# Performance work log

Measured on AMD Instinct MI355X. Metric: run time of the kernel, lower is better.

## Reference

```python
import jax, jax.numpy as jnp
import numpy as np

GRID = 64
ECC = 10.0
ATT_CTR = (3.0, 0.0)
NORM_SIGMA = 0.5


def _grids():
    coords = jnp.linspace(-ECC, ECC, GRID, dtype=jnp.float32)
    X, Y = jnp.meshgrid(coords, coords)          # (64,64)
    RF_X = X.reshape(-1)                         # (4096,) one RF center per grid point
    RF_Y = Y.reshape(-1)
    return X, Y, RF_X, RF_Y


def _fields(X, Y, RF_X, RF_Y, sigma):
    # Batched Gaussian fields: (64,64,4096), each normalized to unit sum.
    d2 = (X[:, :, None] - RF_X) ** 2 + (Y[:, :, None] - RF_Y) ** 2
    g = jnp.exp(-d2 / (2.0 * sigma ** 2))
    return g / jnp.sum(g, axis=(0, 1), keepdims=True)


def setup_inputs() -> dict:
    key = jax.random.key(0)
    ks = jax.random.split(key, 2)
    stim = jax.random.uniform(ks[0], (GRID, GRID, 256), dtype=jnp.float32)
    return {
        "stim": stim,
        "prf_sigma_scale_factor": jnp.float32(0.2),
        "attention_field_sigma": jnp.float32(2.0),
        "attention_field_gain": jnp.float32(4.0),
        "suppressive_surround_sigma_factor": jnp.float32(3.0),
        "summation_field_sigma_factor": jnp.float32(2.0),
    }


def reference(stim, prf_sigma_scale_factor, attention_field_sigma,
              attention_field_gain, suppressive_surround_sigma_factor,
              summation_field_sigma_factor):
    X, Y, RF_X, RF_Y = _grids()
    if stim.ndim != 3:
        stim = stim[:, :, None]

    # Attention field: unnormalized Gaussian, flattened, gain*g + 1.
    att = jnp.exp(-((X - ATT_CTR[0]) ** 2 + (Y - ATT_CTR[1]) ** 2)
                  / (2.0 * attention_field_sigma ** 2)).reshape(-1)  # (4096,)
    attfield = attention_field_gain * att + 1.0

    rf_sigma = 0.07 + prf_sigma_scale_factor * jnp.sqrt(RF_X ** 2 + RF_Y ** 2)  # (4096,)

    receptive_field = _fields(X, Y, RF_X, RF_Y, rf_sigma)                                  # (64,64,4096)
    suppressive_surround = _fields(X, Y, RF_X, RF_Y, rf_sigma * suppressive_surround_sigma_factor).reshape(GRID * GRID, -1)
    summation_field = _fields(X, Y, RF_X, RF_Y, rf_sigma * summation_field_sigma_factor).reshape(GRID * GRID, -1)

    stimulus_drive = jnp.einsum('ijk,ija->ka', receptive_field, stim)   # (4096, a)
    numerator = stimulus_drive * attfield[:, None]                      # (4096, a)
    surroundresponse = suppressive_surround.T @ numerator               # (4096, a)
    predicted_neural = numerator / (surroundresponse + NORM_SIGMA)
    predicted_voxel = summation_field.T @ predicted_neural
    # voxel_lookup_indices is identity (voxeldata=None), so lookups are no-ops.
    return (numerator, surroundresponse, predicted_neural, predicted_voxel)
```

## Files before the change

kernel.cpp:

```cpp
#include <hip/hip_runtime.h>
#include <hip/hip_bf16.h>
#include <math.h>

#define NP 4096
#define NA 256

typedef unsigned short ushort_t;
typedef __attribute__((ext_vector_type(8))) short short8;
typedef __attribute__((ext_vector_type(4))) float f32x4;
typedef __attribute__((ext_vector_type(8))) unsigned short ushort8v;

__device__ __forceinline__ ushort_t f2bf(float x) {
    __hip_bfloat16 h = __float2bfloat16(x);
    return *reinterpret_cast<ushort_t*>(&h);
}
__device__ __forceinline__ float bf2f(ushort_t u) {
    unsigned x = ((unsigned)u) << 16;
    return __builtin_bit_cast(float, x);
}

__global__ __launch_bounds__(512)
void setup_all(const float* __restrict__ stim,
               const float* __restrict__ pscale,
               const float* __restrict__ pasig,
               const float* __restrict__ pagain,
               const float* __restrict__ pssf,
               const float* __restrict__ psff,
               ushort_t* __restrict__ stimT,
               ushort_t* __restrict__ gxbI,
               float* __restrict__ gy2I,
               float* __restrict__ attI)
{
    __shared__ float lt[64 * 68];
    const int t = threadIdx.x;
    const int bx = blockIdx.x;
    const float step = 20.0f / 63.0f;

    if (bx < 256) {
        const int g0 = (bx & 63) * 64, a0 = (bx >> 6) * 64;
        const int gr = t >> 3, ar = (t & 7) * 8;
        *(f32x4*)&lt[gr * 68 + ar]     = *(const f32x4*)&stim[(size_t)(g0 + gr) * NA + a0 + ar];
        *(f32x4*)&lt[gr * 68 + ar + 4] = *(const f32x4*)&stim[(size_t)(g0 + gr) * NA + a0 + ar + 4];
        __syncthreads();
        const int a = t >> 3, c8 = (t & 7) * 8;
        ushort8v u;
        #pragma unroll
        for (int i = 0; i < 8; ++i) u[i] = f2bf(lt[(c8 + i) * 68 + a]);
        *(ushort8v*)&stimT[(size_t)(a0 + a) * NP + g0 + c8] = u;
    } else {
        const int b    = bx - 256;
        const int f    = b >> 6;
        const int pblk = b & 63;
        const int w    = t >> 6;
        const int l    = t & 63;
        const float sc_scale = pscale[0];
        const float fac = (f == 0) ? 1.0f : (f == 1 ? pssf[0] : psff[0]);
        const float coord = -10.0f + step * (float)l;
        ushort_t* gxb = gxbI + ((size_t)f * 64 + pblk) * 4096;
        float*    gy2 = gy2I + ((size_t)f * 64 + pblk) * 4096;

        #pragma unroll
        for (int i = 0; i < 8; ++i) {
            const int pl = w * 8 + i, p = pblk * 64 + pl;
            float cx = -10.0f + step * (float)(p & 63);
            float cy = -10.0f + step * (float)(p >> 6);
            float sg = (0.07f + sc_scale * sqrtf(cx * cx + cy * cy)) * fac;
            float inv = 1.0f / (2.0f * sg * sg);
            float dx = coord - cx, dy = coord - cy;
            float ex = expf(-dx * dx * inv);
            float ey = expf(-dy * dy * inv);
            float sx = ex, sy = ey;
            #pragma unroll
            for (int o = 32; o > 0; o >>= 1) {
                sx += __shfl_xor(sx, o);
                sy += __shfl_xor(sy, o);
            }
            gxb[pl * 64 + l] = f2bf(ex / sx);
            gy2[l * 64 + (((pl & 15) * 4) ^ ((l & 7) << 3)) + (pl >> 4)] = ey / sy;
            if (f == 0 && l == 0) {
                float asig = pasig[0];
                float d2 = (cx - 3.0f) * (cx - 3.0f) + cy * cy;
                attI[p] = pagain[0] * expf(-d2 / (2.0f * asig * asig)) + 1.0f;
            }
        }
    }
}

template <int MODE>
__global__ __launch_bounds__(512)
void field_gemm(const ushort_t* __restrict__ bT,
                const ushort_t* __restrict__ gxbF,
                const float* __restrict__ gy2F,
                const float* __restrict__ attI,
                const float* __restrict__ num,
                float* __restrict__ C,
                float* __restrict__ C2,
                ushort_t* __restrict__ CT,
                const ushort_t* __restrict__ numTsrc)
{
    __shared__ __align__(16) unsigned char smem[147712];
    ushort_t* lB   = (ushort_t*)smem;
    float*    lgy2 = (float*)(smem + 131072);
    float*    latt = (float*)(smem + 147456);

    const int t    = threadIdx.x;
    const int w    = t >> 6;
    const int l    = t & 63;
    const int asub = w >> 1;
    const int kh   = w & 1;
    const int r16  = l & 15;
    const int q    = l >> 4;
    const int srow  = l >> 3;
    const int sslot = (l & 7) ^ (srow & 7);
    const int base_w = kh * 4096 + asub * 1024;

    const int v    = blockIdx.x;
    const int lid  = (v & 7) * 32 + (v >> 3);
    const int pblk = lid & 63;
    const int p0   = pblk * 64;
    const int a0   = (lid >> 6) * 64;

#define STAGE(buf, tn)                                                         \
    _Pragma("unroll")                                                          \
    for (int h = 0; h < 2; ++h) {                                              \
        const ushort_t* src = bT + (size_t)(a0 + asub * 16 + h * 8 + srow) * NP\
                              + (2 * (tn) + kh) * 64 + sslot * 8;              \
        ushort_t* dst = lB + (buf) * 8192 + base_w + h * 512;                  \
        __builtin_amdgcn_global_load_lds(                                      \
            (const __attribute__((address_space(1))) unsigned int*)src,        \
            (__attribute__((address_space(3))) unsigned int*)dst, 16, 0, 0);   \
    }

    STAGE(0, 0); STAGE(1, 1); STAGE(2, 2);
    STAGE(3, 3); STAGE(4, 4); STAGE(5, 5);

    {
        const float* gsrc = gy2F + (size_t)pblk * 4096;
        #pragma unroll
        for (int r = 0; r < 2; ++r) {
            const float* src = gsrc + (w * 2 + r) * 256 + l * 4;
            float* dst = lgy2 + (w * 2 + r) * 256;
            __builtin_amdgcn_global_load_lds(
                (const __attribute__((address_space(1))) unsigned int*)src,
                (__attribute__((address_space(3))) unsigned int*)dst, 16, 0, 0);
        }
    }
    if (MODE == 0 && w == 0) {
        const float* src = attI + p0 + l;
        __builtin_amdgcn_global_load_lds(
            (const __attribute__((address_space(1))) unsigned int*)src,
            (__attribute__((address_space(3))) unsigned int*)latt, 4, 0, 0);
    }

    const ushort_t* gxb = gxbF + (size_t)pblk * 4096;
    short8 gxf[4][2];
    #pragma unroll
    for (int pt = 0; pt < 4; ++pt) {
        const int row = pt * 16 + r16;
        gxf[pt][0] = *(const short8*)&gxb[row * 64 + q * 8];
        gxf[pt][1] = *(const short8*)&gxb[row * 64 + 32 + q * 8];
    }

    __syncthreads();

    const int bo0 = r16 * 64 + ((q ^ (r16 & 7)) * 8);
    const int bo1 = r16 * 64 + (((4 + q) ^ (r16 & 7)) * 8);

    f32x4 acc[4];
    #pragma unroll
    for (int pt = 0; pt < 4; ++pt) acc[pt] = (f32x4){0.f, 0.f, 0.f, 0.f};

    short8 Aa0, Aa1, Ab0, Ab1;
    f32x4 s4a, s4b;
    {
        const ushort_t* bb0 = lB + base_w;
        Aa0 = *(const short8*)(bb0 + bo0);
        Aa1 = *(const short8*)(bb0 + bo1);
        const int gi0 = kh;
        s4a = *(const f32x4*)(lgy2 + gi0 * 64 + ((r16 * 4) ^ ((gi0 & 7) << 3)));
    }

#define STEP(TT, VM, CA0, CA1, CS4, NA0, NA1, NS4, PRE, ST)                    \
    {                                                                          \
        const int tt_k = (TT);                                                 \
        asm volatile("s_waitcnt vmcnt(" #VM ")" ::: "memory");                 \
        if (PRE) {                                                             \
            const ushort_t* bbn = lB + ((tt_k + 1) & 7) * 8192 + base_w;       \
            NA0 = *(const short8*)(bbn + bo0);                                 \
            NA1 = *(const short8*)(bbn + bo1);                                 \
            const int gin = 2 * (tt_k + 1) + kh;                               \
            NS4 = *(const f32x4*)(lgy2 + gin * 64 +                            \
                                  ((r16 * 4) ^ ((gin & 7) << 3)));             \
        }                                                                      \
        if (ST) { STAGE((tt_k + 6) & 7, tt_k + 6); }                           \
        __builtin_amdgcn_s_setprio(1);                                         \
        _Pragma("unroll")                                                      \
        for (int pt = 0; pt < 4; ++pt) {                                       \
            f32x4 tmp = (f32x4){0.f, 0.f, 0.f, 0.f};                           \
            tmp = __builtin_amdgcn_mfma_f32_16x16x32_bf16(CA0, gxf[pt][0], tmp, 0, 0, 0); \
            tmp = __builtin_amdgcn_mfma_f32_16x16x32_bf16(CA1, gxf[pt][1], tmp, 0, 0, 0); \
            float sc = CS4[pt];                                                \
            acc[pt] += tmp * sc;                                               \
        }                                                                      \
        __builtin_amdgcn_s_setprio(0);                                         \
    }

    #pragma unroll
    for (int pi = 0; pi < 13; ++pi) {
        STEP(2 * pi,     8, Aa0, Aa1, s4a, Ab0, Ab1, s4b, 1, 1);
        STEP(2 * pi + 1, 8, Ab0, Ab1, s4b, Aa0, Aa1, s4a, 1, 1);
    }
    STEP(26, 8, Aa0, Aa1, s4a, Ab0, Ab1, s4b, 1, 0);
    STEP(27, 6, Ab0, Ab1, s4b, Aa0, Aa1, s4a, 1, 0);
    STEP(28, 4, Aa0, Aa1, s4a, Ab0, Ab1, s4b, 1, 0);
    STEP(29, 2, Ab0, Ab1, s4b, Aa0, Aa1, s4a, 1, 0);
    STEP(30, 0, Aa0, Aa1, s4a, Ab0, Ab1, s4b, 1, 0);
    STEP(31, 0, Ab0, Ab1, s4b, Aa0, Aa1, s4a, 0, 0);
#undef STEP
#undef STAGE

    __syncthreads();
    float* lred_ap = (float*)smem;
    float* lred_pa = (float*)(smem + 34816);

    const int a_base = asub * 16 + q * 4;
    #pragma unroll
    for (int pt = 0; pt < 4; ++pt) {
        const int p_idx = pt * 16 + r16;
        *(f32x4*)&lred_pa[(kh * 64 + p_idx) * 68 + a_base] = acc[pt];
        #pragma unroll
        for (int r = 0; r < 4; ++r)
            lred_ap[(kh * 64 + a_base + r) * 68 + p_idx] = acc[pt][r];
    }
    __syncthreads();

    if (MODE != 2) {
        const int aL = t >> 3, p8 = (t & 7) * 8;
        f32x4 s0 = *(f32x4*)&lred_ap[aL * 68 + p8] +
                   *(f32x4*)&lred_ap[(64 + aL) * 68 + p8];
        f32x4 s1 = *(f32x4*)&lred_ap[aL * 68 + p8 + 4] +
                   *(f32x4*)&lred_ap[(64 + aL) * 68 + p8 + 4];
        ushort8v cv;
        if (MODE == 0) {
            f32x4 t0 = *(f32x4*)&latt[p8];
            f32x4 t1 = *(f32x4*)&latt[p8 + 4];
            s0 *= t0; s1 *= t1;
            #pragma unroll
            for (int r = 0; r < 4; ++r) {
                cv[r] = f2bf(s0[r]);
                cv[4 + r] = f2bf(s1[r]);
            }
        } else {
            ushort8v nt = *(const ushort8v*)&numTsrc[(size_t)(a0 + aL) * NP + p0 + p8];
            #pragma unroll
            for (int r = 0; r < 4; ++r) {
                cv[r] = f2bf(bf2f(nt[r]) / (s0[r] + 0.5f));
                cv[4 + r] = f2bf(bf2f(nt[4 + r]) / (s1[r] + 0.5f));
            }
        }
        *(ushort8v*)&CT[(size_t)(a0 + aL) * NP + p0 + p8] = cv;
    }

    {
        const int pL = t >> 3, a8 = (t & 7) * 8;
        f32x4 s0 = *(f32x4*)&lred_pa[pL * 68 + a8] +
                   *(f32x4*)&lred_pa[(64 + pL) * 68 + a8];
        f32x4 s1 = *(f32x4*)&lred_pa[pL * 68 + a8 + 4] +
                   *(f32x4*)&lred_pa[(64 + pL) * 68 + a8 + 4];
        float* cbase = C + (size_t)(p0 + pL) * NA + a0 + a8;
        if (MODE == 0) {
            float att = latt[pL];
            s0 *= att; s1 *= att;
            *(f32x4*)cbase = s0;
            *(f32x4*)(cbase + 4) = s1;
        } else if (MODE == 1) {
            *(f32x4*)cbase = s0;
            *(f32x4*)(cbase + 4) = s1;
            const float* nb = num + (size_t)(p0 + pL) * NA + a0 + a8;
            f32x4 n0 = *(const f32x4*)nb;
            f32x4 n1 = *(const f32x4*)(nb + 4);
            f32x4 o0 = n0 / (s0 + 0.5f);
            f32x4 o1 = n1 / (s1 + 0.5f);
            float* c2 = C2 + (size_t)(p0 + pL) * NA + a0 + a8;
            *(f32x4*)c2 = o0;
            *(f32x4*)(c2 + 4) = o1;
        } else {
            *(f32x4*)cbase = s0;
            *(f32x4*)(cbase + 4) = s1;
        }
    }
}

extern "C" void kernel_launch(void* const* d_in, const int* in_sizes, int n_in,
                              void* d_out, int out_size, void* d_ws, size_t ws_size,
                              hipStream_t stream)
{
    const float* stim   = (const float*)d_in[0];
    const float* pscale = (const float*)d_in[1];
    const float* pasig  = (const float*)d_in[2];
    const float* pagain = (const float*)d_in[3];
    const float* pssf   = (const float*)d_in[4];
    const float* psff   = (const float*)d_in[5];

    float* out  = (float*)d_out;
    float* num  = out;
    float* surr = out + (size_t)NP * NA;
    float* pn   = out + 2 * (size_t)NP * NA;
    float* pv   = out + 3 * (size_t)NP * NA;

    ushort_t* stimT = (ushort_t*)d_ws;
    ushort_t* numT  = stimT + (size_t)NA * NP;
    ushort_t* pnT   = numT + (size_t)NA * NP;
    ushort_t* gxbI  = pnT + (size_t)NA * NP;
    float*    gy2I  = (float*)(gxbI + (size_t)3 * 64 * 4096);
    float*    attI  = gy2I + (size_t)3 * 64 * 4096;

    setup_all<<<448, 512, 0, stream>>>(stim, pscale, pasig, pagain, pssf, psff,
                                       stimT, gxbI, gy2I, attI);

    const ushort_t* gx0 = gxbI;
    const ushort_t* gx1 = gxbI + (size_t)64 * 4096;
    const ushort_t* gx2 = gxbI + (size_t)128 * 4096;
    const float*    gy0 = gy2I;
    const float*    gy1 = gy2I + (size_t)64 * 4096;
    const float*    gy2 = gy2I + (size_t)128 * 4096;

    field_gemm<0><<<256, 512, 0, stream>>>(stimT, gx0, gy0, attI, nullptr,
                                           num, nullptr, numT, nullptr);
    field_gemm<1><<<256, 512, 0, stream>>>(numT, gx1, gy1, attI, num,
                                           surr, pn, pnT, numT);
    field_gemm<2><<<256, 512, 0, stream>>>(pnT, gx2, gy2, attI, nullptr,
                                           pv, nullptr, nullptr, nullptr);
}
```

Measured before the change: 57.42 us.

## Split K four ways across 16 waves per block in field GEMM

Doubles the field_gemm block to 1024 threads so that four wave groups split the 4096-long reduction instead of two, each running 16 pipeline steps instead of 32. The staging ring shrinks from 8 buffers to 4 larger ones with a prefetch depth of 3, and the LDS reduction now sums four partial tiles, with each thread writing 4-wide outputs. The aim is more latency hiding and a shorter serial K loop per wave, since only 256 blocks are launched. The cost is a shallower prefetch pipeline, a larger cross-wave reduction, and more register and LDS pressure under the 1024-thread launch bound.

```diff
diff --git a/kernel.cpp b/kernel.cpp
--- a/kernel.cpp
+++ b/kernel.cpp
@@ -8,6 +8,7 @@
 typedef unsigned short ushort_t;
 typedef __attribute__((ext_vector_type(8))) short short8;
 typedef __attribute__((ext_vector_type(4))) float f32x4;
+typedef __attribute__((ext_vector_type(4))) unsigned short ushort4v;
 typedef __attribute__((ext_vector_type(8))) unsigned short ushort8v;
 
 __device__ __forceinline__ ushort_t f2bf(float x) {
@@ -87,7 +88,7 @@
 }
 
 template <int MODE>
-__global__ __launch_bounds__(512)
+__global__ __launch_bounds__(1024)
 void field_gemm(const ushort_t* __restrict__ bT,
                 const ushort_t* __restrict__ gxbF,
                 const float* __restrict__ gy2F,
@@ -106,13 +107,13 @@
     const int t    = threadIdx.x;
     const int w    = t >> 6;
     const int l    = t & 63;
-    const int asub = w >> 1;
-    const int kh   = w & 1;
+    const int asub = w >> 2;
+    const int kq   = w & 3;
     const int r16  = l & 15;
     const int q    = l >> 4;
     const int srow  = l >> 3;
     const int sslot = (l & 7) ^ (srow & 7);
-    const int base_w = kh * 4096 + asub * 1024;
+    const int base_w = kq * 4096 + asub * 1024;
 
     const int v    = blockIdx.x;
     const int lid  = (v & 7) * 32 + (v >> 3);
@@ -124,26 +125,21 @@
     _Pragma("unroll")                                                          \
     for (int h = 0; h < 2; ++h) {                                              \
         const ushort_t* src = bT + (size_t)(a0 + asub * 16 + h * 8 + srow) * NP\
-                              + (2 * (tn) + kh) * 64 + sslot * 8;              \
-        ushort_t* dst = lB + (buf) * 8192 + base_w + h * 512;                  \
+                              + (4 * (tn) + kq) * 64 + sslot * 8;              \
+        ushort_t* dst = lB + (buf) * 16384 + base_w + h * 512;                 \
         __builtin_amdgcn_global_load_lds(                                      \
             (const __attribute__((address_space(1))) unsigned int*)src,        \
             (__attribute__((address_space(3))) unsigned int*)dst, 16, 0, 0);   \
     }
 
     STAGE(0, 0); STAGE(1, 1); STAGE(2, 2);
-    STAGE(3, 3); STAGE(4, 4); STAGE(5, 5);
 
     {
-        const float* gsrc = gy2F + (size_t)pblk * 4096;
-        #pragma unroll
-        for (int r = 0; r < 2; ++r) {
-            const float* src = gsrc + (w * 2 + r) * 256 + l * 4;
-            float* dst = lgy2 + (w * 2 + r) * 256;
-            __builtin_amdgcn_global_load_lds(
-                (const __attribute__((address_space(1))) unsigned int*)src,
-                (__attribute__((address_space(3))) unsigned int*)dst, 16, 0, 0);
-        }
+        const float* src = gy2F + (size_t)pblk * 4096 + w * 256 + l * 4;
+        float* dst = lgy2 + w * 256;
+        __builtin_amdgcn_global_load_lds(
+            (const __attribute__((address_space(1))) unsigned int*)src,
+            (__attribute__((address_space(3))) unsigned int*)dst, 16, 0, 0);
     }
     if (MODE == 0 && w == 0) {
         const float* src = attI + p0 + l;
@@ -176,7 +172,7 @@
         const ushort_t* bb0 = lB + base_w;
         Aa0 = *(const short8*)(bb0 + bo0);
         Aa1 = *(const short8*)(bb0 + bo1);
-        const int gi0 = kh;
+        const int gi0 = kq;
         s4a = *(const f32x4*)(lgy2 + gi0 * 64 + ((r16 * 4) ^ ((gi0 & 7) << 3)));
     }
 
@@ -185,14 +181,14 @@
         const int tt_k = (TT);                                                 \
         asm volatile("s_waitcnt vmcnt(" #VM ")" ::: "memory");                 \
         if (PRE) {                                                             \
-            const ushort_t* bbn = lB + ((tt_k + 1) & 7) * 8192 + base_w;       \
+            const ushort_t* bbn = lB + ((tt_k + 1) & 3) * 16384 + base_w;      \
             NA0 = *(const short8*)(bbn + bo0);                                 \
             NA1 = *(const short8*)(bbn + bo1);                                 \
-            const int gin = 2 * (tt_k + 1) + kh;                               \
+            const int gin = 4 * (tt_k + 1) + kq;                               \
             NS4 = *(const f32x4*)(lgy2 + gin * 64 +                            \
                                   ((r16 * 4) ^ ((gin & 7) << 3)));             \
         }                                                                      \
-        if (ST) { STAGE((tt_k + 6) & 7, tt_k + 6); }                           \
+        if (ST) { STAGE((tt_k + 3) & 3, tt_k + 3); }                           \
         __builtin_amdgcn_s_setprio(1);                                         \
         _Pragma("unroll")                                                      \
         for (int pt = 0; pt < 4; ++pt) {                                       \
@@ -206,87 +202,69 @@
     }
 
     #pragma unroll
-    for (int pi = 0; pi < 13; ++pi) {
-        STEP(2 * pi,     8, Aa0, Aa1, s4a, Ab0, Ab1, s4b, 1, 1);
-        STEP(2 * pi + 1, 8, Ab0, Ab1, s4b, Aa0, Aa1, s4a, 1, 1);
-    }
-    STEP(26, 8, Aa0, Aa1, s4a, Ab0, Ab1, s4b, 1, 0);
-    STEP(27, 6, Ab0, Ab1, s4b, Aa0, Aa1, s4a, 1, 0);
-    STEP(28, 4, Aa0, Aa1, s4a, Ab0, Ab1, s4b, 1, 0);
-    STEP(29, 2, Ab0, Ab1, s4b, Aa0, Aa1, s4a, 1, 0);
-    STEP(30, 0, Aa0, Aa1, s4a, Ab0, Ab1, s4b, 1, 0);
-    STEP(31, 0, Ab0, Ab1, s4b, Aa0, Aa1, s4a, 0, 0);
+    for (int pi = 0; pi < 6; ++pi) {
+        STEP(2 * pi,     2, Aa0, Aa1, s4a, Ab0, Ab1, s4b, 1, 1);
+        STEP(2 * pi + 1, 2, Ab0, Ab1, s4b, Aa0, Aa1, s4a, 1, 1);
+    }
+    STEP(12, 2, Aa0, Aa1, s4a, Ab0, Ab1, s4b, 1, 1);
+    STEP(13, 2, Ab0, Ab1, s4b, Aa0, Aa1, s4a, 1, 0);
+    STEP(14, 0, Aa0, Aa1, s4a, Ab0, Ab1, s4b, 1, 0);
+    STEP(15, 0, Ab0, Ab1, s4b, Aa0, Aa1, s4a, 0, 0);
 #undef STEP
 #undef STAGE
 
     __syncthreads();
-    float* lred_ap = (float*)smem;
-    float* lred_pa = (float*)(smem + 34816);
+    float* lred_pa = (float*)smem;
+    float* lred_ap = (float*)(smem + 69632);
 
     const int a_base = asub * 16 + q * 4;
     #pragma unroll
     for (int pt = 0; pt < 4; ++pt) {
         const int p_idx = pt * 16 + r16;
-        *(f32x4*)&lred_pa[(kh * 64 + p_idx) * 68 + a_base] = acc[pt];
+        *(f32x4*)&lred_pa[(kq * 64 + p_idx) * 68 + a_base] = acc[pt];
         #pragma unroll
         for (int r = 0; r < 4; ++r)
-            lred_ap[(kh * 64 + a_base + r) * 68 + p_idx] = acc[pt][r];
+            lred_ap[(kq * 64 + a_base + r) * 68 + p_idx] = acc[pt][r];
     }
     __syncthreads();
 
     if (MODE != 2) {
-        const int aL = t >> 3, p8 = (t & 7) * 8;
-        f32x4 s0 = *(f32x4*)&lred_ap[aL * 68 + p8] +
-                   *(f32x4*)&lred_ap[(64 + aL) * 68 + p8];
-        f32x4 s1 = *(f32x4*)&lred_ap[aL * 68 + p8 + 4] +
-                   *(f32x4*)&lred_ap[(64 + aL) * 68 + p8 + 4];
-        ushort8v cv;
+        const int aL = t >> 4, p4 = (t & 15) * 4;
+        f32x4 s0 = *(f32x4*)&lred_ap[aL * 68 + p4] +
+                   *(f32x4*)&lred_ap[(64 + aL) * 68 + p4] +
+                   *(f32x4*)&lred_ap[(128 + aL) * 68 + p4] +
+                   *(f32x4*)&lred_ap[(192 + aL) * 68 + p4];
+        ushort4v cv;
         if (MODE == 0) {
-            f32x4 t0 = *(f32x4*)&latt[p8];
-            f32x4 t1 = *(f32x4*)&latt[p8 + 4];
-            s0 *= t0; s1 *= t1;
+            s0 *= *(f32x4*)&latt[p4];
             #pragma unroll
-            for (int r = 0; r < 4; ++r) {
-                cv[r] = f2bf(s0[r]);
-                cv[4 + r] = f2bf(s1[r]);
-            }
+            for (int r = 0; r < 4; ++r) cv[r] = f2bf(s0[r]);
         } else {
-            ushort8v nt = *(const ushort8v*)&numTsrc[(size_t)(a0 + aL) * NP + p0 + p8];
+            ushort4v nt = *(const ushort4v*)&numTsrc[(size_t)(a0 + aL) * NP + p0 + p4];
             #pragma unroll
-            for (int r = 0; r < 4; ++r) {
+            for (int r = 0; r < 4; ++r)
                 cv[r] = f2bf(bf2f(nt[r]) / (s0[r] + 0.5f));
-                cv[4 + r] = f2bf(bf2f(nt[4 + r]) / (s1[r] + 0.5f));
-            }
         }
-        *(ushort8v*)&CT[(size_t)(a0 + aL) * NP + p0 + p8] = cv;
+        *(ushort4v*)&CT[(size_t)(a0 + aL) * NP + p0 + p4] = cv;
     }
 
     {
-        const int pL = t >> 3, a8 = (t & 7) * 8;
-        f32x4 s0 = *(f32x4*)&lred_pa[pL * 68 + a8] +
-                   *(f32x4*)&lred_pa[(64 + pL) * 68 + a8];
-        f32x4 s1 = *(f32x4*)&lred_pa[pL * 68 + a8 + 4] +
-                   *(f32x4*)&lred_pa[(64 + pL) * 68 + a8 + 4];
-        float* cbase = C + (size_t)(p0 + pL) * NA + a0 + a8;
+        const int pL = t >> 4, a4 = (t & 15) * 4;
+        f32x4 s0 = *(f32x4*)&lred_pa[pL * 68 + a4] +
+                   *(f32x4*)&lred_pa[(64 + pL) * 68 + a4] +
+                   *(f32x4*)&lred_pa[(128 + pL) * 68 + a4] +
+                   *(f32x4*)&lred_pa[(192 + pL) * 68 + a4];
+        float* cbase = C + (size_t)(p0 + pL) * NA + a0 + a4;
         if (MODE == 0) {
-            float att = latt[pL];
-            s0 *= att; s1 *= att;
+            s0 *= latt[pL];
             *(f32x4*)cbase = s0;
-            *(f32x4*)(cbase + 4) = s1;
         } else if (MODE == 1) {
             *(f32x4*)cbase = s0;
-            *(f32x4*)(cbase + 4) = s1;
-            const float* nb = num + (size_t)(p0 + pL) * NA + a0 + a8;
-            f32x4 n0 = *(const f32x4*)nb;
-            f32x4 n1 = *(const f32x4*)(nb + 4);
+            f32x4 n0 = *(const f32x4*)(num + (size_t)(p0 + pL) * NA + a0 + a4);
             f32x4 o0 = n0 / (s0 + 0.5f);
-            f32x4 o1 = n1 / (s1 + 0.5f);
-            float* c2 = C2 + (size_t)(p0 + pL) * NA + a0 + a8;
-            *(f32x4*)c2 = o0;
-            *(f32x4*)(c2 + 4) = o1;
+            *(f32x4*)(C2 + (size_t)(p0 + pL) * NA + a0 + a4) = o0;
         } else {
             *(f32x4*)cbase = s0;
-            *(f32x4*)(cbase + 4) = s1;
         }
     }
 }
@@ -325,10 +303,10 @@
     const float*    gy1 = gy2I + (size_t)64 * 4096;
     const float*    gy2 = gy2I + (size_t)128 * 4096;
 
-    field_gemm<0><<<256, 512, 0, stream>>>(stimT, gx0, gy0, attI, nullptr,
-                                           num, nullptr, numT, nullptr);
-    field_gemm<1><<<256, 512, 0, stream>>>(numT, gx1, gy1, attI, num,
-                                           surr, pn, pnT, numT);
-    field_gemm<2><<<256, 512, 0, stream>>>(pnT, gx2, gy2, attI, nullptr,
-                                           pv, nullptr, nullptr, nullptr);
-}
+    field_gemm<0><<<256, 1024, 0, stream>>>(stimT, gx0, gy0, attI, nullptr,
+                                            num, nullptr, numT, nullptr);
+    field_gemm<1><<<256, 1024, 0, stream>>>(numT, gx1, gy1, attI, num,
+                                            surr, pn, pnT, numT);
+    field_gemm<2><<<256, 1024, 0, stream>>>(pnT, gx2, gy2, attI, nullptr,
+                                            pv, nullptr, nullptr, nullptr);
+}
```

After: 61.57 us. +7.2%, slower.

## Load B operand directly from global into registers, drop LDS staging ring

Applied to the files above, without the earlier changes.

Replaces the 8-buffer LDS ring fed by global_load_lds with direct per-lane global loads of the bT operand into a 4-deep register rotation consumed by the MFMAs. This removes the LDS write/read traffic, the manual vmcnt waits and one barrier, and shrinks shared memory from about 148KB to 86KB, which could allow more resident blocks. In exchange each lane issues strided global loads with less prefetch depth, so latency hiding now depends on the compiler's scheduling and on the cache.

```diff
diff --git a/kernel.cpp b/kernel.cpp
--- a/kernel.cpp
+++ b/kernel.cpp
@@ -98,10 +98,11 @@
                 ushort_t* __restrict__ CT,
                 const ushort_t* __restrict__ numTsrc)
 {
-    __shared__ __align__(16) unsigned char smem[147712];
-    ushort_t* lB   = (ushort_t*)smem;
-    float*    lgy2 = (float*)(smem + 131072);
-    float*    latt = (float*)(smem + 147456);
+    __shared__ __align__(16) unsigned char smem[86272];
+    float* lred_ap = (float*)smem;
+    float* lred_pa = (float*)(smem + 34816);
+    float* lgy2    = (float*)(smem + 69632);
+    float* latt    = (float*)(smem + 86016);
 
     const int t    = threadIdx.x;
     const int w    = t >> 6;
@@ -110,29 +111,12 @@
     const int kh   = w & 1;
     const int r16  = l & 15;
     const int q    = l >> 4;
-    const int srow  = l >> 3;
-    const int sslot = (l & 7) ^ (srow & 7);
-    const int base_w = kh * 4096 + asub * 1024;
 
     const int v    = blockIdx.x;
     const int lid  = (v & 7) * 32 + (v >> 3);
     const int pblk = lid & 63;
     const int p0   = pblk * 64;
     const int a0   = (lid >> 6) * 64;
-
-#define STAGE(buf, tn)                                                         \
-    _Pragma("unroll")                                                          \
-    for (int h = 0; h < 2; ++h) {                                              \
-        const ushort_t* src = bT + (size_t)(a0 + asub * 16 + h * 8 + srow) * NP\
-                              + (2 * (tn) + kh) * 64 + sslot * 8;              \
-        ushort_t* dst = lB + (buf) * 8192 + base_w + h * 512;                  \
-        __builtin_amdgcn_global_load_lds(                                      \
-            (const __attribute__((address_space(1))) unsigned int*)src,        \
-            (__attribute__((address_space(3))) unsigned int*)dst, 16, 0, 0);   \
-    }
-
-    STAGE(0, 0); STAGE(1, 1); STAGE(2, 2);
-    STAGE(3, 3); STAGE(4, 4); STAGE(5, 5);
 
     {
         const float* gsrc = gy2F + (size_t)pblk * 4096;
@@ -161,38 +145,34 @@
         gxf[pt][1] = *(const short8*)&gxb[row * 64 + 32 + q * 8];
     }
 
+    const ushort_t* gbase = bT + (size_t)(a0 + asub * 16 + r16) * NP + q * 8;
+#define GLOAD(D0, D1, TT) {                                                    \
+        const int goff = (2 * (TT) + kh) * 64;                                 \
+        D0 = *(const short8*)(gbase + goff);                                   \
+        D1 = *(const short8*)(gbase + goff + 32); }
+
+    short8 pa0, pa1, pb0, pb1, pc0, pc1, pd0, pd1;
+    GLOAD(pa0, pa1, 0); GLOAD(pb0, pb1, 1);
+    GLOAD(pc0, pc1, 2); GLOAD(pd0, pd1, 3);
+
     __syncthreads();
-
-    const int bo0 = r16 * 64 + ((q ^ (r16 & 7)) * 8);
-    const int bo1 = r16 * 64 + (((4 + q) ^ (r16 & 7)) * 8);
 
     f32x4 acc[4];
     #pragma unroll
     for (int pt = 0; pt < 4; ++pt) acc[pt] = (f32x4){0.f, 0.f, 0.f, 0.f};
 
-    short8 Aa0, Aa1, Ab0, Ab1;
     f32x4 s4a, s4b;
-    {
-        const ushort_t* bb0 = lB + base_w;
-        Aa0 = *(const short8*)(bb0 + bo0);
-        Aa1 = *(const short8*)(bb0 + bo1);
-        const int gi0 = kh;
+    {   const int gi0 = kh;
         s4a = *(const f32x4*)(lgy2 + gi0 * 64 + ((r16 * 4) ^ ((gi0 & 7) << 3)));
     }
 
-#define STEP(TT, VM, CA0, CA1, CS4, NA0, NA1, NS4, PRE, ST)                    \
+#define STEP(TT, CA0, CA1, CS4, NS4, PRE, LD)                                  \
     {                                                                          \
-        const int tt_k = (TT);                                                 \
-        asm volatile("s_waitcnt vmcnt(" #VM ")" ::: "memory");                 \
         if (PRE) {                                                             \
-            const ushort_t* bbn = lB + ((tt_k + 1) & 7) * 8192 + base_w;       \
-            NA0 = *(const short8*)(bbn + bo0);                                 \
-            NA1 = *(const short8*)(bbn + bo1);                                 \
-            const int gin = 2 * (tt_k + 1) + kh;                               \
+            const int gin = 2 * ((TT) + 1) + kh;                               \
             NS4 = *(const f32x4*)(lgy2 + gin * 64 +                            \
                                   ((r16 * 4) ^ ((gin & 7) << 3)));             \
         }                                                                      \
-        if (ST) { STAGE((tt_k + 6) & 7, tt_k + 6); }                           \
         __builtin_amdgcn_s_setprio(1);                                         \
         _Pragma("unroll")                                                      \
         for (int pt = 0; pt < 4; ++pt) {                                       \
@@ -203,25 +183,22 @@
             acc[pt] += tmp * sc;                                               \
         }                                                                      \
         __builtin_amdgcn_s_setprio(0);                                         \
-    }
-
-    #pragma unroll
-    for (int pi = 0; pi < 13; ++pi) {
-        STEP(2 * pi,     8, Aa0, Aa1, s4a, Ab0, Ab1, s4b, 1, 1);
-        STEP(2 * pi + 1, 8, Ab0, Ab1, s4b, Aa0, Aa1, s4a, 1, 1);
-    }
-    STEP(26, 8, Aa0, Aa1, s4a, Ab0, Ab1, s4b, 1, 0);
-    STEP(27, 6, Ab0, Ab1, s4b, Aa0, Aa1, s4a, 1, 0);
-    STEP(28, 4, Aa0, Aa1, s4a, Ab0, Ab1, s4b, 1, 0);
-    STEP(29, 2, Ab0, Ab1, s4b, Aa0, Aa1, s4a, 1, 0);
-    STEP(30, 0, Aa0, Aa1, s4a, Ab0, Ab1, s4b, 1, 0);
-    STEP(31, 0, Ab0, Ab1, s4b, Aa0, Aa1, s4a, 0, 0);
+        if (LD) { GLOAD(CA0, CA1, (TT) + 4); }                                 \
+    }
+
+    for (int g4 = 0; g4 < 7; ++g4) {
+        const int b4 = 4 * g4;
+        STEP(b4 + 0, pa0, pa1, s4a, s4b, 1, 1);
+        STEP(b4 + 1, pb0, pb1, s4b, s4a, 1, 1);
+        STEP(b4 + 2, pc0, pc1, s4a, s4b, 1, 1);
+        STEP(b4 + 3, pd0, pd1, s4b, s4a, 1, 1);
+    }
+    STEP(28, pa0, pa1, s4a, s4b, 1, 0);
+    STEP(29, pb0, pb1, s4b, s4a, 1, 0);
+    STEP(30, pc0, pc1, s4a, s4b, 1, 0);
+    STEP(31, pd0, pd1, s4b, s4a, 0, 0);
 #undef STEP
-#undef STAGE
-
-    __syncthreads();
-    float* lred_ap = (float*)smem;
-    float* lred_pa = (float*)(smem + 34816);
+#undef GLOAD
 
     const int a_base = asub * 16 + q * 4;
     #pragma unroll
```

Result: slower. 78.21 us (+36.2%).
